# Performance work log

Hardware: AMD Instinct MI355X
Metric: run time of the kernel (lower is better)

The kernel has to match this reference:

```python
import jax, jax.numpy as jnp
import numpy as np

B, D, U, R, H, ND = 32768, 1024, 1024, 4, 16, 11


def setup_inputs() -> dict:
    key = jax.random.key(0)
    ks = jax.random.split(key, 12)
    s = 0.02
    return {
        "x": jax.random.normal(ks[0], (B, D), dtype=jnp.float32),
        "domain_indicator": jax.random.randint(ks[1], (B, 1), 0, ND, dtype=jnp.int32),
        "kernel": jax.random.normal(ks[2], (D, U), dtype=jnp.float32) * s,
        "bias": jnp.zeros((U,), dtype=jnp.float32),
        "a_kernel": jax.random.normal(ks[3], (ND, D, R), dtype=jnp.float32) * s,
        "b_kernel": jax.random.normal(ks[4], (ND, R, U), dtype=jnp.float32) * s,
        "domain_bias": jnp.zeros((ND, U), dtype=jnp.float32),
        "WQ": jax.random.normal(ks[5], (R, H), dtype=jnp.float32) * s,
        "WK": jax.random.normal(ks[6], (R, H), dtype=jnp.float32) * s,
        "WV": jax.random.normal(ks[7], (R, H), dtype=jnp.float32) * s,
        "linear": jax.random.normal(ks[8], (H, R), dtype=jnp.float32) * s,
        "factor": jax.random.normal(ks[9], (1, ND), dtype=jnp.float32) * s,
    }


def reference(x, domain_indicator, kernel, bias, a_kernel, b_kernel,
              domain_bias, WQ, WK, WV, linear, factor):
    # Base dense path (dropout inactive at inference)
    out = x @ kernel + bias  # [B, U]

    # Per-domain LoRA-A gather (domains 1..10) and projection: [B, 10, R]
    dA = jnp.einsum('bd,ndr->bnr', x, a_kernel[1:11])

    # Tiny self-attention over the 10 domain projections
    Q = dA @ WQ  # [B, 10, H]
    Kt = dA @ WK
    V = dA @ WV
    scale = 1.0 / jnp.sqrt(jnp.float32(H))
    A = jax.nn.softmax(jnp.einsum('bnh,bmh->bnm', Q, Kt) * scale, axis=-1)
    O = jnp.einsum('bnm,bmh->bnh', A, V) @ linear  # [B, 10, R]

    # Sum over domains -> shared LoRA latent [B, R]
    dom = jnp.sum(O, axis=1)

    # Per-domain LoRA-B expansion: [B, 10, U]
    dB = jnp.einsum('br,nru->bnu', dom, b_kernel[1:11])

    # Domain mixture weights (softmax over all n_domain, cols 1..10 used)
    w = jax.nn.softmax(factor, axis=-1)[0, 1:11]  # [10]
    dout = jnp.einsum('bnu,n->bu', dB, w)  # [B, U]

    # Domain bias from the indicator of the first row
    idx = domain_indicator[0, 0]
    dout = dout + domain_bias[idx]

    return jax.nn.relu(out + dout)
```

## Files before the change

### kernel.cpp

```cpp
#include <hip/hip_runtime.h>
#include <hip/hip_bf16.h>


typedef float f32x4 __attribute__((ext_vector_type(4)));
typedef short s16x8 __attribute__((ext_vector_type(8)));
typedef unsigned int u32x4 __attribute__((ext_vector_type(4)));

#define WS_DOM    0u
#define WS_BEFF   524288u
#define WS_BIAS   540672u
#define WS_G      544768u
#define WS_M      545024u
#define WS_ACATT  545280u
#define WS_KB     679936u
#define WS_XB     2777088u

__device__ __forceinline__ unsigned short f2bf(float f) {
  unsigned int u = __builtin_bit_cast(unsigned int, f);
  u += 0x7fffu + ((u >> 16) & 1u);
  return (unsigned short)(u >> 16);
}
__device__ __forceinline__ unsigned int f2bf2(float a, float b) {
  return (unsigned int)f2bf(a) | ((unsigned int)f2bf(b) << 16);
}

__device__ __forceinline__ void gload_lds16(const void* g, void* l) {
  __builtin_amdgcn_global_load_lds((const __attribute__((address_space(1))) void*)g,
                                   (__attribute__((address_space(3))) void*)l, 16, 0, 0);
}

__global__ void prep1(const float* __restrict__ factor, const float* __restrict__ WQ,
                      const float* __restrict__ WK, const float* __restrict__ WV,
                      const float* __restrict__ linear, const float* __restrict__ bias,
                      const float* __restrict__ domain_bias, const float* __restrict__ b_kernel,
                      const int* __restrict__ dom_ind, float* __restrict__ ws_f) {
  __shared__ float wsm[10];
  const int t = threadIdx.x;
  float* G    = ws_f + (WS_G >> 2);
  float* M    = ws_f + (WS_M >> 2);
  float* beff = ws_f + (WS_BEFF >> 2);
  float* btot = ws_f + (WS_BIAS >> 2);
  if (t == 0) {
    float f[11], mx = -1e30f;
    for (int i = 0; i < 11; i++) { f[i] = factor[i]; mx = fmaxf(mx, f[i]); }
    float s = 0.f;
    for (int i = 0; i < 11; i++) { f[i] = expf(f[i] - mx); s += f[i]; }
    float inv = 1.0f / s;
    for (int i = 0; i < 10; i++) wsm[i] = f[i + 1] * inv;
  }
  if (t < 16) {
    int r = t >> 2, c = t & 3;
    float g = 0.f, m = 0.f;
    for (int h = 0; h < 16; h++) {
      g += WQ[r * 16 + h] * WK[c * 16 + h];
      m += WV[r * 16 + h] * linear[h * 4 + c];
    }
    G[t] = 0.25f * g;
    M[t] = m;
  }
  __syncthreads();
  const int idx = dom_ind[0];
  for (int u = t; u < 1024; u += 256) btot[u] = bias[u] + domain_bias[idx * 1024 + u];
  for (int i = t; i < 4096; i += 256) {
    int r = i >> 10, u = i & 1023;
    float s = 0.f;
    for (int n = 0; n < 10; n++) s += wsm[n] * b_kernel[(1 + n) * 4096 + r * 1024 + u];
    beff[i] = s;
  }
}

__global__ void prep2(const float* __restrict__ a_kernel, unsigned short* __restrict__ acatt) {
  const int i = blockIdx.x * 256 + threadIdx.x;
  const int c = i >> 10, d = i & 1023;
  float v = 0.0f;
  if (c < 40) v = a_kernel[(1 + (c >> 2)) * 4096 + d * 4 + (c & 3)];
  acatt[i] = f2bf(v);
}

__global__ void transK(const float* __restrict__ kern, unsigned short* __restrict__ kb) {
  __shared__ float tile[32][33];
  const int t = threadIdx.x;
  const int kt = blockIdx.x >> 5, nt = blockIdx.x & 31;
  const int k0 = kt << 5, n0 = nt << 5;
  const int row = t >> 5, col = t & 31;
#pragma unroll
  for (int i = 0; i < 4; i++)
    tile[row + i * 8][col] = kern[(k0 + row + i * 8) * 1024 + n0 + col];
  __syncthreads();
  const int nrow = t >> 3, kq = t & 7;
  uint2 pv;
  pv.x = f2bf2(tile[kq * 4 + 0][nrow], tile[kq * 4 + 1][nrow]);
  pv.y = f2bf2(tile[kq * 4 + 2][nrow], tile[kq * 4 + 3][nrow]);
  *reinterpret_cast<uint2*>(&kb[(n0 + nrow) * 1024 + k0 + kq * 4]) = pv;
}

template <bool WRITEXB>
__launch_bounds__(256, 2)
__global__ void stageA(const float* __restrict__ x, const unsigned short* __restrict__ acatt,
                       const float* __restrict__ ws_f, float* __restrict__ dom,
                       unsigned short* __restrict__ xb) {
  __shared__ unsigned short As[64 * 64];
  __shared__ unsigned short Bs[64 * 64];
  __shared__ float dAs[64][45];
  const int t = threadIdx.x;
  const int w = t >> 6, l = t & 63;
  const int rows0 = blockIdx.x << 6;
  const int lr = l & 15, kg = l >> 4;
  const f32x4 zero4 = {0.f, 0.f, 0.f, 0.f};
  f32x4 acc[3]; acc[0] = zero4; acc[1] = zero4; acc[2] = zero4;

#pragma unroll 1
  for (int kc = 0; kc < 16; kc++) {
    if (kc) __syncthreads();
#pragma unroll
    for (int i = 0; i < 2; i++) {
      int segid = i * 256 + t;
      int c = segid >> 3, ks = segid & 7;
      gload_lds16(acatt + c * 1024 + (kc << 6) + ((ks ^ (c & 7)) << 3), Bs + segid * 8);
    }
#pragma unroll
    for (int i = 0; i < 2; i++) {
      int segid = i * 256 + t;
      int row = segid >> 3, ks = segid & 7;
      const float* gp = x + (rows0 + row) * 1024 + (kc << 6) + (ks << 3);
      f32x4 v0 = *reinterpret_cast<const f32x4*>(gp);
      f32x4 v1 = *reinterpret_cast<const f32x4*>(gp + 4);
      u32x4 o = { f2bf2(v0[0], v0[1]), f2bf2(v0[2], v0[3]),
                  f2bf2(v1[0], v1[1]), f2bf2(v1[2], v1[3]) };
      *reinterpret_cast<u32x4*>(As + row * 64 + ((ks ^ (row & 7)) << 3)) = o;
      if (WRITEXB)
        *reinterpret_cast<u32x4*>(xb + (rows0 + row) * 1024 + (kc << 6) + (ks << 3)) = o;
    }
    __syncthreads();
#pragma unroll
    for (int kh = 0; kh < 2; kh++) {
      const int cp = (kh << 2) + kg;
      const int arow = (w << 4) + lr;
      s16x8 av = *reinterpret_cast<const s16x8*>(As + arow * 64 + ((cp ^ (arow & 7)) << 3));
#pragma unroll
      for (int nf = 0; nf < 3; nf++) {
        int brow = (nf << 4) + lr;
        s16x8 bv = *reinterpret_cast<const s16x8*>(Bs + brow * 64 + ((cp ^ (brow & 7)) << 3));
        acc[nf] = __builtin_amdgcn_mfma_f32_16x16x32_bf16(av, bv, acc[nf], 0, 0, 0);
      }
    }
  }
  __syncthreads();
#pragma unroll
  for (int nf = 0; nf < 3; nf++) {
    int col = (nf << 4) + lr;
    if (col < 40) {
#pragma unroll
      for (int j = 0; j < 4; j++)
        dAs[(w << 4) + (kg << 2) + j][col] = acc[nf][j];
    }
  }
  __syncthreads();
  if (l < 16) {
    const int row = (w << 4) + l;
    const float* Gp = ws_f + (WS_G >> 2);
    const float* Mp = ws_f + (WS_M >> 2);
    float dA[10][4];
#pragma unroll
    for (int m = 0; m < 10; m++)
#pragma unroll
      for (int r = 0; r < 4; r++) dA[m][r] = dAs[row][(m << 2) + r];
    float Gv[16], Mv[16];
#pragma unroll
    for (int i = 0; i < 16; i++) { Gv[i] = Gp[i]; Mv[i] = Mp[i]; }
    float tm[10][4];
#pragma unroll
    for (int m = 0; m < 10; m++)
#pragma unroll
      for (int r = 0; r < 4; r++)
        tm[m][r] = Gv[(r << 2) + 0] * dA[m][0] + Gv[(r << 2) + 1] * dA[m][1]
                 + Gv[(r << 2) + 2] * dA[m][2] + Gv[(r << 2) + 3] * dA[m][3];
    float cm[10];
#pragma unroll
    for (int m = 0; m < 10; m++) cm[m] = 0.f;
#pragma unroll
    for (int n = 0; n < 10; n++) {
      float sv[10]; float mx = -1e30f;
#pragma unroll
      for (int m = 0; m < 10; m++) {
        float s = dA[n][0] * tm[m][0] + dA[n][1] * tm[m][1]
                + dA[n][2] * tm[m][2] + dA[n][3] * tm[m][3];
        sv[m] = s; mx = fmaxf(mx, s);
      }
      float ssum = 0.f;
#pragma unroll
      for (int m = 0; m < 10; m++) { float e = expf(sv[m] - mx); sv[m] = e; ssum += e; }
      float inv = 1.0f / ssum;
#pragma unroll
      for (int m = 0; m < 10; m++) cm[m] += sv[m] * inv;
    }
    float u0 = 0.f, u1 = 0.f, u2 = 0.f, u3 = 0.f;
#pragma unroll
    for (int m = 0; m < 10; m++) {
      u0 += cm[m] * dA[m][0]; u1 += cm[m] * dA[m][1];
      u2 += cm[m] * dA[m][2]; u3 += cm[m] * dA[m][3];
    }
    f32x4 dv;
#pragma unroll
    for (int rp = 0; rp < 4; rp++)
      dv[rp] = u0 * Mv[rp] + u1 * Mv[4 + rp] + u2 * Mv[8 + rp] + u3 * Mv[12 + rp];
    *reinterpret_cast<f32x4*>(&dom[(rows0 + row) << 2]) = dv;
  }
}

template <bool XB>
__launch_bounds__(256, 3)
__global__ void mainGEMM(const float* __restrict__ x, const unsigned short* __restrict__ xb,
                         const unsigned short* __restrict__ kb,
                         const float* __restrict__ ws_f, float* __restrict__ out) {
  __shared__ unsigned short As[8192];
  __shared__ unsigned short Bs[8192];
  const int t = threadIdx.x;
  const int w = t >> 6, l = t & 63;
  const int b = blockIdx.x;
  const int xcd = b & 7, i6 = b >> 3;
  const int bm = (xcd << 5) + (i6 >> 3), bn = i6 & 7;
  const int rows0 = bm << 7, cols0 = bn << 7;
  const int wr = w >> 1, wc = w & 1;
  const int lr = l & 15, kg = l >> 4;
  const float* dom  = ws_f + (WS_DOM >> 2);
  const float* beff = ws_f + (WS_BEFF >> 2);
  const float* btot = ws_f + (WS_BIAS >> 2);
  const f32x4 zero4 = {0.f, 0.f, 0.f, 0.f};
  f32x4 acc[4][4];
#pragma unroll
  for (int i = 0; i < 4; i++)
#pragma unroll
    for (int j = 0; j < 4; j++) acc[i][j] = zero4;

#pragma unroll 1
  for (int kc = 0; kc < 16; kc++) {
    if (kc) __syncthreads();
#pragma unroll
    for (int i = 0; i < 4; i++) {
      int segid = i * 256 + t;
      int c = segid >> 3, ks = segid & 7;
      gload_lds16(kb + (cols0 + c) * 1024 + (kc << 6) + ((ks ^ (c & 7)) << 3), Bs + segid * 8);
    }
#pragma unroll
    for (int i = 0; i < 4; i++) {
      int segid = i * 256 + t;
      int row = segid >> 3, ks = segid & 7;
      if (XB) {
        gload_lds16(xb + (rows0 + row) * 1024 + (kc << 6) + ((ks ^ (row & 7)) << 3),
                    As + segid * 8);
      } else {
        const float* gp = x + (rows0 + row) * 1024 + (kc << 6) + (ks << 3);
        f32x4 v0 = *reinterpret_cast<const f32x4*>(gp);
        f32x4 v1 = *reinterpret_cast<const f32x4*>(gp + 4);
        u32x4 o = { f2bf2(v0[0], v0[1]), f2bf2(v0[2], v0[3]),
                    f2bf2(v1[0], v1[1]), f2bf2(v1[2], v1[3]) };
        *reinterpret_cast<u32x4*>(As + row * 64 + ((ks ^ (row & 7)) << 3)) = o;
      }
    }
    __syncthreads();
#pragma unroll
    for (int kh = 0; kh < 2; kh++) {
      const int cp = (kh << 2) + kg;
      s16x8 av[4], bv[4];
#pragma unroll
      for (int mf = 0; mf < 4; mf++) {
        int arow = (wr << 6) + (mf << 4) + lr;
        av[mf] = *reinterpret_cast<const s16x8*>(As + arow * 64 + ((cp ^ (arow & 7)) << 3));
      }
#pragma unroll
      for (int nf = 0; nf < 4; nf++) {
        int brow = (wc << 6) + (nf << 4) + lr;
        bv[nf] = *reinterpret_cast<const s16x8*>(Bs + brow * 64 + ((cp ^ (brow & 7)) << 3));
      }
#pragma unroll
      for (int mf = 0; mf < 4; mf++)
#pragma unroll
        for (int nf = 0; nf < 4; nf++)
          acc[mf][nf] = __builtin_amdgcn_mfma_f32_16x16x32_bf16(av[mf], bv[nf], acc[mf][nf], 0, 0, 0);
    }
  }

  float bcv[4], bev[4][4];
#pragma unroll
  for (int nf = 0; nf < 4; nf++) {
    int col = cols0 + (wc << 6) + (nf << 4) + lr;
    bcv[nf] = btot[col];
#pragma unroll
    for (int r = 0; r < 4; r++) bev[nf][r] = beff[r * 1024 + col];
  }
#pragma unroll
  for (int mf = 0; mf < 4; mf++) {
    const int rbase = rows0 + (wr << 6) + (mf << 4) + (kg << 2);
    f32x4 dm[4];
#pragma unroll
    for (int j = 0; j < 4; j++)
      dm[j] = *reinterpret_cast<const f32x4*>(dom + ((rbase + j) << 2));
#pragma unroll
    for (int nf = 0; nf < 4; nf++) {
      const int col = cols0 + (wc << 6) + (nf << 4) + lr;
#pragma unroll
      for (int j = 0; j < 4; j++) {
        float v = acc[mf][nf][j] + bcv[nf]
                + dm[j][0] * bev[nf][0] + dm[j][1] * bev[nf][1]
                + dm[j][2] * bev[nf][2] + dm[j][3] * bev[nf][3];
        out[(rbase + j) * 1024 + col] = fmaxf(v, 0.f);
      }
    }
  }
}

extern "C" void kernel_launch(void* const* d_in, const int* in_sizes, int n_in,
                              void* d_out, int out_size, void* d_ws, size_t ws_size,
                              hipStream_t stream) {
  (void)in_sizes; (void)n_in; (void)out_size;
  const float* x           = (const float*)d_in[0];
  const int*   dom_ind     = (const int*)d_in[1];
  const float* kern        = (const float*)d_in[2];
  const float* bias        = (const float*)d_in[3];
  const float* a_kernel    = (const float*)d_in[4];
  const float* b_kernel    = (const float*)d_in[5];
  const float* domain_bias = (const float*)d_in[6];
  const float* WQ          = (const float*)d_in[7];
  const float* WK          = (const float*)d_in[8];
  const float* WV          = (const float*)d_in[9];
  const float* linear      = (const float*)d_in[10];
  const float* factor      = (const float*)d_in[11];
  float* out = (float*)d_out;
  char* ws = (char*)d_ws;
  float* ws_f = (float*)ws;
  unsigned short* acatt = (unsigned short*)(ws + WS_ACATT);
  unsigned short* kb    = (unsigned short*)(ws + WS_KB);
  unsigned short* xb    = (unsigned short*)(ws + WS_XB);
  float* dom            = (float*)(ws + WS_DOM);
  const bool use_xb = ws_size >= (size_t)WS_XB + (size_t)32768 * 1024 * 2;

  prep1<<<1, 256, 0, stream>>>(factor, WQ, WK, WV, linear, bias, domain_bias, b_kernel, dom_ind, ws_f);
  prep2<<<256, 256, 0, stream>>>(a_kernel, acatt);
  transK<<<1024, 256, 0, stream>>>(kern, kb);
  if (use_xb) {
    stageA<true><<<512, 256, 0, stream>>>(x, acatt, ws_f, dom, xb);
    mainGEMM<true><<<2048, 256, 0, stream>>>(x, xb, kb, ws_f, out);
  } else {
    stageA<false><<<512, 256, 0, stream>>>(x, acatt, ws_f, dom, xb);
    mainGEMM<false><<<2048, 256, 0, stream>>>(x, xb, kb, ws_f, out);
  }
}
```

Measured before the change: 146.2 us.

## Restructure stageA to stage full 32-row x slab in LDS with split-K waves

stageA now processes 32 rows per block with a grid of 1024 blocks. Each block first loads its whole 32x1024 x slab with double-buffered register prefetch, converts it to bf16 into a swizzled 64KB LDS buffer, and writes xb. The per-k-chunk loop with two barriers is removed. The four waves then split the work as 2 row groups x 2 K halves, read the A-projection weights directly from global memory instead of LDS, and sum the two K halves in LDS before the attention step. This cuts synchronisation and raises memory-level parallelism. In exchange the larger LDS footprint lowers occupancy, and the B operand comes from global/L2 with uncoalesced 16-byte reads.

```diff
diff --git a/kernel.cpp b/kernel.cpp
--- a/kernel.cpp
+++ b/kernel.cpp
@@ -99,72 +99,77 @@
 __global__ void stageA(const float* __restrict__ x, const unsigned short* __restrict__ acatt,
                        const float* __restrict__ ws_f, float* __restrict__ dom,
                        unsigned short* __restrict__ xb) {
-  __shared__ unsigned short As[64 * 64];
-  __shared__ unsigned short Bs[64 * 64];
-  __shared__ float dAs[64][45];
+  __shared__ unsigned short As[32 * 1024];
+  __shared__ float dAs[2][32][49];
   const int t = threadIdx.x;
+  const int rows0 = blockIdx.x << 5;
+
+#define SA_LOAD(buf, base)                                                              \
+  _Pragma("unroll")                                                                     \
+  for (int j = 0; j < 8; j++)                                                           \
+    buf[j] = *reinterpret_cast<const f32x4*>(x + (size_t)(rows0 + (base) + j) * 1024 + (t << 2));
+#define SA_PROC(buf, base)                                                              \
+  _Pragma("unroll")                                                                     \
+  for (int j = 0; j < 8; j++) {                                                         \
+    const int i = (base) + j;                                                           \
+    uint2 p;                                                                            \
+    p.x = f2bf2(buf[j][0], buf[j][1]);                                                  \
+    p.y = f2bf2(buf[j][2], buf[j][3]);                                                  \
+    *reinterpret_cast<uint2*>(As + (((i << 10) + (t << 2)) ^ ((i & 7) << 3))) = p;      \
+    if (WRITEXB)                                                                        \
+      *reinterpret_cast<uint2*>(xb + (size_t)(rows0 + i) * 1024 + (t << 2)) = p;        \
+  }
+  {
+    f32x4 va[8], vb[8];
+    SA_LOAD(va, 0)
+    SA_LOAD(vb, 8)
+    SA_PROC(va, 0)
+    SA_LOAD(va, 16)
+    SA_PROC(vb, 8)
+    SA_LOAD(vb, 24)
+    SA_PROC(va, 16)
+    SA_PROC(vb, 24)
+  }
+  __syncthreads();
+
   const int w = t >> 6, l = t & 63;
-  const int rows0 = blockIdx.x << 6;
+  const int rg = w >> 1, kh = w & 1;
   const int lr = l & 15, kg = l >> 4;
+  const int arow = (rg << 4) + lr;
   const f32x4 zero4 = {0.f, 0.f, 0.f, 0.f};
   f32x4 acc[3]; acc[0] = zero4; acc[1] = zero4; acc[2] = zero4;
-
-#pragma unroll 1
-  for (int kc = 0; kc < 16; kc++) {
-    if (kc) __syncthreads();
-#pragma unroll
-    for (int i = 0; i < 2; i++) {
-      int segid = i * 256 + t;
-      int c = segid >> 3, ks = segid & 7;
-      gload_lds16(acatt + c * 1024 + (kc << 6) + ((ks ^ (c & 7)) << 3), Bs + segid * 8);
-    }
-#pragma unroll
-    for (int i = 0; i < 2; i++) {
-      int segid = i * 256 + t;
-      int row = segid >> 3, ks = segid & 7;
-      const float* gp = x + (rows0 + row) * 1024 + (kc << 6) + (ks << 3);
-      f32x4 v0 = *reinterpret_cast<const f32x4*>(gp);
-      f32x4 v1 = *reinterpret_cast<const f32x4*>(gp + 4);
-      u32x4 o = { f2bf2(v0[0], v0[1]), f2bf2(v0[2], v0[3]),
-                  f2bf2(v1[0], v1[1]), f2bf2(v1[2], v1[3]) };
-      *reinterpret_cast<u32x4*>(As + row * 64 + ((ks ^ (row & 7)) << 3)) = o;
-      if (WRITEXB)
-        *reinterpret_cast<u32x4*>(xb + (rows0 + row) * 1024 + (kc << 6) + (ks << 3)) = o;
-    }
-    __syncthreads();
-#pragma unroll
-    for (int kh = 0; kh < 2; kh++) {
-      const int cp = (kh << 2) + kg;
-      const int arow = (w << 4) + lr;
-      s16x8 av = *reinterpret_cast<const s16x8*>(As + arow * 64 + ((cp ^ (arow & 7)) << 3));
-#pragma unroll
-      for (int nf = 0; nf < 3; nf++) {
-        int brow = (nf << 4) + lr;
-        s16x8 bv = *reinterpret_cast<const s16x8*>(Bs + brow * 64 + ((cp ^ (brow & 7)) << 3));
-        acc[nf] = __builtin_amdgcn_mfma_f32_16x16x32_bf16(av, bv, acc[nf], 0, 0, 0);
-      }
+#pragma unroll 4
+  for (int s = 0; s < 16; s++) {
+    const int kelem = (kh << 9) + (s << 5) + (kg << 3);
+    s16x8 av = *reinterpret_cast<const s16x8*>(As + (((arow << 10) + kelem) ^ ((arow & 7) << 3)));
+#pragma unroll
+    for (int nf = 0; nf < 3; nf++) {
+      const int brow = (nf << 4) + lr;
+      s16x8 bv = *reinterpret_cast<const s16x8*>(acatt + brow * 1024 + kelem);
+      acc[nf] = __builtin_amdgcn_mfma_f32_16x16x32_bf16(av, bv, acc[nf], 0, 0, 0);
+    }
+  }
+#pragma unroll
+  for (int nf = 0; nf < 3; nf++) {
+    const int col = (nf << 4) + lr;
+    if (col < 40) {
+#pragma unroll
+      for (int j = 0; j < 4; j++)
+        dAs[kh][(rg << 4) + (kg << 2) + j][col] = acc[nf][j];
     }
   }
   __syncthreads();
-#pragma unroll
-  for (int nf = 0; nf < 3; nf++) {
-    int col = (nf << 4) + lr;
-    if (col < 40) {
-#pragma unroll
-      for (int j = 0; j < 4; j++)
-        dAs[(w << 4) + (kg << 2) + j][col] = acc[nf][j];
-    }
-  }
-  __syncthreads();
-  if (l < 16) {
-    const int row = (w << 4) + l;
+
+  if (t < 32) {
+    const int row = t;
     const float* Gp = ws_f + (WS_G >> 2);
     const float* Mp = ws_f + (WS_M >> 2);
     float dA[10][4];
 #pragma unroll
     for (int m = 0; m < 10; m++)
 #pragma unroll
-      for (int r = 0; r < 4; r++) dA[m][r] = dAs[row][(m << 2) + r];
+      for (int r = 0; r < 4; r++)
+        dA[m][r] = dAs[0][row][(m << 2) + r] + dAs[1][row][(m << 2) + r];
     float Gv[16], Mv[16];
 #pragma unroll
     for (int i = 0; i < 16; i++) { Gv[i] = Gp[i]; Mv[i] = Mp[i]; }
@@ -339,10 +344,10 @@
   prep2<<<256, 256, 0, stream>>>(a_kernel, acatt);
   transK<<<1024, 256, 0, stream>>>(kern, kb);
   if (use_xb) {
-    stageA<true><<<512, 256, 0, stream>>>(x, acatt, ws_f, dom, xb);
+    stageA<true><<<1024, 256, 0, stream>>>(x, acatt, ws_f, dom, xb);
     mainGEMM<true><<<2048, 256, 0, stream>>>(x, xb, kb, ws_f, out);
   } else {
-    stageA<false><<<512, 256, 0, stream>>>(x, acatt, ws_f, dom, xb);
+    stageA<false><<<1024, 256, 0, stream>>>(x, acatt, ws_f, dom, xb);
     mainGEMM<false><<<2048, 256, 0, stream>>>(x, xb, kb, ws_f, out);
   }
 }
```

Result: slower. 158.8 us (+8.6%).

## Restructure stageA into 16-row blocks with split-K across warps

Applied to the files above, without the earlier changes.

stageA now handles 16 rows per block instead of 64 and is launched with four times as many blocks. Each block loads its whole 16x1024 x slice into LDS in one pass, converts it to bf16 and optionally writes xb. Each of the four warps then computes a quarter of the K range, reading the LoRA-A weights directly from global memory rather than staging them in LDS, and the partial results are summed through LDS. This drops the per-chunk sync loop and is meant to raise parallelism and occupancy, at the cost of 16 live f32x4 registers per thread and repeated global reads of acatt by every block.

```diff
diff --git a/kernel.cpp b/kernel.cpp
--- a/kernel.cpp
+++ b/kernel.cpp
@@ -95,76 +95,66 @@
 }
 
 template <bool WRITEXB>
-__launch_bounds__(256, 2)
+__launch_bounds__(256, 3)
 __global__ void stageA(const float* __restrict__ x, const unsigned short* __restrict__ acatt,
                        const float* __restrict__ ws_f, float* __restrict__ dom,
                        unsigned short* __restrict__ xb) {
-  __shared__ unsigned short As[64 * 64];
-  __shared__ unsigned short Bs[64 * 64];
-  __shared__ float dAs[64][45];
+  __shared__ unsigned short As[16 * 1024];
+  __shared__ float dAs[4][16][49];
   const int t = threadIdx.x;
+  const int rows0 = blockIdx.x << 4;
+
+  f32x4 v[16];
+#pragma unroll
+  for (int j = 0; j < 16; j++)
+    v[j] = *reinterpret_cast<const f32x4*>(x + (size_t)(rows0 + j) * 1024 + (t << 2));
+#pragma unroll
+  for (int j = 0; j < 16; j++) {
+    uint2 p;
+    p.x = f2bf2(v[j][0], v[j][1]);
+    p.y = f2bf2(v[j][2], v[j][3]);
+    if (WRITEXB)
+      *reinterpret_cast<uint2*>(xb + (size_t)(rows0 + j) * 1024 + (t << 2)) = p;
+    *reinterpret_cast<uint2*>(As + (((j << 10) + (t << 2)) ^ ((j & 7) << 3))) = p;
+  }
+  __syncthreads();
+
   const int w = t >> 6, l = t & 63;
-  const int rows0 = blockIdx.x << 6;
   const int lr = l & 15, kg = l >> 4;
   const f32x4 zero4 = {0.f, 0.f, 0.f, 0.f};
   f32x4 acc[3]; acc[0] = zero4; acc[1] = zero4; acc[2] = zero4;
-
-#pragma unroll 1
-  for (int kc = 0; kc < 16; kc++) {
-    if (kc) __syncthreads();
-#pragma unroll
-    for (int i = 0; i < 2; i++) {
-      int segid = i * 256 + t;
-      int c = segid >> 3, ks = segid & 7;
-      gload_lds16(acatt + c * 1024 + (kc << 6) + ((ks ^ (c & 7)) << 3), Bs + segid * 8);
-    }
-#pragma unroll
-    for (int i = 0; i < 2; i++) {
-      int segid = i * 256 + t;
-      int row = segid >> 3, ks = segid & 7;
-      const float* gp = x + (rows0 + row) * 1024 + (kc << 6) + (ks << 3);
-      f32x4 v0 = *reinterpret_cast<const f32x4*>(gp);
-      f32x4 v1 = *reinterpret_cast<const f32x4*>(gp + 4);
-      u32x4 o = { f2bf2(v0[0], v0[1]), f2bf2(v0[2], v0[3]),
-                  f2bf2(v1[0], v1[1]), f2bf2(v1[2], v1[3]) };
-      *reinterpret_cast<u32x4*>(As + row * 64 + ((ks ^ (row & 7)) << 3)) = o;
-      if (WRITEXB)
-        *reinterpret_cast<u32x4*>(xb + (rows0 + row) * 1024 + (kc << 6) + (ks << 3)) = o;
-    }
-    __syncthreads();
-#pragma unroll
-    for (int kh = 0; kh < 2; kh++) {
-      const int cp = (kh << 2) + kg;
-      const int arow = (w << 4) + lr;
-      s16x8 av = *reinterpret_cast<const s16x8*>(As + arow * 64 + ((cp ^ (arow & 7)) << 3));
-#pragma unroll
-      for (int nf = 0; nf < 3; nf++) {
-        int brow = (nf << 4) + lr;
-        s16x8 bv = *reinterpret_cast<const s16x8*>(Bs + brow * 64 + ((cp ^ (brow & 7)) << 3));
-        acc[nf] = __builtin_amdgcn_mfma_f32_16x16x32_bf16(av, bv, acc[nf], 0, 0, 0);
-      }
+#pragma unroll
+  for (int s = 0; s < 8; s++) {
+    const int kelem = (w << 8) + (s << 5) + (kg << 3);
+    s16x8 av = *reinterpret_cast<const s16x8*>(As + (((lr << 10) + kelem) ^ ((lr & 7) << 3)));
+#pragma unroll
+    for (int nf = 0; nf < 3; nf++) {
+      s16x8 bv = *reinterpret_cast<const s16x8*>(acatt + ((nf << 4) + lr) * 1024 + kelem);
+      acc[nf] = __builtin_amdgcn_mfma_f32_16x16x32_bf16(av, bv, acc[nf], 0, 0, 0);
+    }
+  }
+#pragma unroll
+  for (int nf = 0; nf < 3; nf++) {
+    const int col = (nf << 4) + lr;
+    if (col < 40) {
+#pragma unroll
+      for (int j = 0; j < 4; j++)
+        dAs[w][(kg << 2) + j][col] = acc[nf][j];
     }
   }
   __syncthreads();
-#pragma unroll
-  for (int nf = 0; nf < 3; nf++) {
-    int col = (nf << 4) + lr;
-    if (col < 40) {
-#pragma unroll
-      for (int j = 0; j < 4; j++)
-        dAs[(w << 4) + (kg << 2) + j][col] = acc[nf][j];
-    }
-  }
-  __syncthreads();
-  if (l < 16) {
-    const int row = (w << 4) + l;
+
+  if (t < 16) {
+    const int row = t;
     const float* Gp = ws_f + (WS_G >> 2);
     const float* Mp = ws_f + (WS_M >> 2);
     float dA[10][4];
 #pragma unroll
     for (int m = 0; m < 10; m++)
 #pragma unroll
-      for (int r = 0; r < 4; r++) dA[m][r] = dAs[row][(m << 2) + r];
+      for (int r = 0; r < 4; r++)
+        dA[m][r] = dAs[0][row][(m << 2) + r] + dAs[1][row][(m << 2) + r]
+                 + dAs[2][row][(m << 2) + r] + dAs[3][row][(m << 2) + r];
     float Gv[16], Mv[16];
 #pragma unroll
     for (int i = 0; i < 16; i++) { Gv[i] = Gp[i]; Mv[i] = Mp[i]; }
@@ -339,10 +329,10 @@
   prep2<<<256, 256, 0, stream>>>(a_kernel, acatt);
   transK<<<1024, 256, 0, stream>>>(kern, kb);
   if (use_xb) {
-    stageA<true><<<512, 256, 0, stream>>>(x, acatt, ws_f, dom, xb);
+    stageA<true><<<2048, 256, 0, stream>>>(x, acatt, ws_f, dom, xb);
     mainGEMM<true><<<2048, 256, 0, stream>>>(x, xb, kb, ws_f, out);
   } else {
-    stageA<false><<<512, 256, 0, stream>>>(x, acatt, ws_f, dom, xb);
+    stageA<false><<<2048, 256, 0, stream>>>(x, acatt, ws_f, dom, xb);
     mainGEMM<false><<<2048, 256, 0, stream>>>(x, xb, kb, ws_f, out);
   }
 }
```

New measurement: 181.3 us. 1.24x slower.
